# Kernel optimization log

Measured on AMD Instinct MI355X. Metric: run time of the kernel, lower is better.

The kernel has to match this reference:

```python
import jax, jax.numpy as jnp
import numpy as np

NUM_HEADS = 16
HEAD_SIZE = 64
D_MODEL = NUM_HEADS * HEAD_SIZE  # 1024


def setup_inputs() -> dict:
    key = jax.random.key(0)
    ks = jax.random.split(key, 12)
    B, S = 4, 2048
    q = jax.random.normal(ks[0], (B, S, D_MODEL), dtype=jnp.float32)
    k = jax.random.normal(ks[1], (B, S, D_MODEL), dtype=jnp.float32)
    v = jax.random.normal(ks[2], (B, S, D_MODEL), dtype=jnp.float32)
    w = jax.random.uniform(ks[3], (B, S), dtype=jnp.float32)
    scale = 1.0 / np.sqrt(D_MODEL)
    Wq = jax.random.normal(ks[4], (D_MODEL, D_MODEL), dtype=jnp.float32) * scale
    Wk = jax.random.normal(ks[5], (D_MODEL, D_MODEL), dtype=jnp.float32) * scale
    Wv = jax.random.normal(ks[6], (D_MODEL, D_MODEL), dtype=jnp.float32) * scale
    Wo = jax.random.normal(ks[7], (D_MODEL, D_MODEL), dtype=jnp.float32) * scale
    bq = jnp.zeros((D_MODEL,), jnp.float32)
    bk = jnp.zeros((D_MODEL,), jnp.float32)
    bv = jnp.zeros((D_MODEL,), jnp.float32)
    bo = jnp.zeros((D_MODEL,), jnp.float32)
    return {"q": q, "k": k, "v": v, "w": w,
            "Wq": Wq, "bq": bq, "Wk": Wk, "bk": bk,
            "Wv": Wv, "bv": bv, "Wo": Wo, "bo": bo}


def reference(q, k, v, w, Wq, bq, Wk, bk, Wv, bv, Wo, bo):
    B, S, _ = q.shape
    H, Dh = NUM_HEADS, HEAD_SIZE

    def split_heads(x):  # [B,S,D] -> [B,H,S,Dh]
        return x.reshape(B, -1, H, Dh).transpose(0, 2, 1, 3)

    q_h = split_heads(q @ Wq + bq)
    k_h = split_heads(k @ Wk + bk)
    v_h = split_heads(v @ Wv + bv)

    # [B,H,Sq,Sk]
    score = jnp.einsum('bhqd,bhkd->bhqk', q_h, k_h) / jnp.sqrt(
        jnp.asarray(Dh, jnp.float32))
    # weighted unnormalized softmax: exp(score)*w / sum (no max subtraction,
    # faithful to original)
    exp_score = jnp.exp(score) * w[:, None, None, :]
    attn = exp_score / (jnp.sum(exp_score, axis=-1, keepdims=True) + 1e-12)

    context = jnp.einsum('bhqk,bhkd->bhqd', attn, v_h)  # [B,H,S,Dh]
    context = context.transpose(0, 2, 1, 3).reshape(B, -1, H * Dh)
    return context @ Wo + bo
```

## Files before the change

### kernel.cpp

```cpp
#include <hip/hip_runtime.h>
#include <hip/hip_bf16.h>

typedef __bf16 bf16x8 __attribute__((ext_vector_type(8)));
typedef float f32x4 __attribute__((ext_vector_type(4)));
typedef float f32x8 __attribute__((ext_vector_type(8)));
typedef float f32x16 __attribute__((ext_vector_type(16)));
typedef unsigned short u16;
typedef unsigned int u32;

#define SB 4
#define SS 2048
#define SD 1024
#define SH 16
#define SDH 64

__device__ __forceinline__ u16 f2bf(float f) {
  union { float f; u32 u; } x; x.f = f;
  u32 r = (x.u + 0x7FFFu + ((x.u >> 16) & 1u)) >> 16;
  return (u16)r;
}

__device__ __forceinline__ void gl_lds16(const void* g, void* l) {
  __builtin_amdgcn_global_load_lds(
      (__attribute__((address_space(1))) void*)g,
      (__attribute__((address_space(3))) void*)l, 16, 0, 0);
}

__global__ void cast_bf16_kernel(const float* __restrict__ in,
                                 u32* __restrict__ out, int n8) {
  int i = blockIdx.x * blockDim.x + threadIdx.x;
  if (i >= n8) return;
  const float4* inp = (const float4*)in;
  float4 a = inp[2 * i], b = inp[2 * i + 1];
  uint4 o;
  asm("v_cvt_pk_bf16_f32 %0, %1, %2" : "=v"(o.x) : "v"(a.x), "v"(a.y));
  asm("v_cvt_pk_bf16_f32 %0, %1, %2" : "=v"(o.y) : "v"(a.z), "v"(a.w));
  asm("v_cvt_pk_bf16_f32 %0, %1, %2" : "=v"(o.z) : "v"(b.x), "v"(b.y));
  asm("v_cvt_pk_bf16_f32 %0, %1, %2" : "=v"(o.w) : "v"(b.z), "v"(b.w));
  ((uint4*)out)[i] = o;
}

__global__ void log2w_kernel(const float* __restrict__ w,
                             float* __restrict__ lwg) {
  int i = blockIdx.x * 256 + threadIdx.x;
  lwg[i] = __builtin_amdgcn_logf(w[i]);
}

__global__ void transpose_cast_kernel(const float* __restrict__ W0,
                                      const float* __restrict__ W1,
                                      const float* __restrict__ W2,
                                      const float* __restrict__ W3,
                                      u16* __restrict__ T0,
                                      u16* __restrict__ T1,
                                      u16* __restrict__ T2,
                                      u16* __restrict__ T3) {
  __shared__ float t[32][33];
  int z = blockIdx.z;
  const float* W = (z == 0) ? W0 : (z == 1) ? W1 : (z == 2) ? W2 : W3;
  u16* Wt = (z == 0) ? T0 : (z == 1) ? T1 : (z == 2) ? T2 : T3;
  int bx = blockIdx.x, by = blockIdx.y;
  int tx = threadIdx.x, ty = threadIdx.y;
#pragma unroll
  for (int j = 0; j < 32; j += 8)
    t[ty + j][tx] = W[(size_t)(by * 32 + ty + j) * SD + bx * 32 + tx];
  __syncthreads();
#pragma unroll
  for (int j = 0; j < 32; j += 8)
    Wt[(size_t)(bx * 32 + ty + j) * SD + by * 32 + tx] = f2bf(t[tx][ty + j]);
}

template <int MODE>
__global__ __launch_bounds__(256, 2)
void gemm_bt(const u16* __restrict__ A, const u16* __restrict__ Bt,
             const float* __restrict__ bias, void* __restrict__ Out,
             int M, int N, int K) {
  __shared__ u16 Asl[2][128 * 64];
  __shared__ u16 Bsl[2][128 * 64];
  const int ntile = N >> 7;
  int bid = blockIdx.x;
  bid = (bid & 7) * ((int)gridDim.x >> 3) + (bid >> 3);
  int m0 = (bid / ntile) * 128, n0 = (bid % ntile) * 128;
  int tid = threadIdx.x;
  int lane = tid & 63, wv = tid >> 6;
  int wr = wv >> 1, wc = wv & 1;

  auto stage = [&](int buf, int k0) {
#pragma unroll
    for (int it = 0; it < 4; ++it) {
      int c = tid + it * 256;
      int row = c >> 3, sl = c & 7;
      int ssl = sl ^ (row & 7);
      gl_lds16(A + (size_t)(m0 + row) * K + k0 + ssl * 8,
               (char*)&Asl[buf][0] + c * 16);
      gl_lds16(Bt + (size_t)(n0 + row) * K + k0 + ssl * 8,
               (char*)&Bsl[buf][0] + c * 16);
    }
  };

  f32x4 acc[4][4] = {};
  stage(0, 0);

  int nk = K >> 6;
  for (int kt = 0; kt < nk; ++kt) {
    int buf = kt & 1;
    if (kt + 1 < nk) {
      stage(buf ^ 1, (kt + 1) << 6);
      asm volatile("s_waitcnt vmcnt(8) lgkmcnt(0)" ::: "memory");
    } else {
      asm volatile("s_waitcnt vmcnt(0) lgkmcnt(0)" ::: "memory");
    }
    __builtin_amdgcn_s_barrier();
#pragma unroll
    for (int kk = 0; kk < 2; ++kk) {
      bf16x8 af[4], bfr[4];
#pragma unroll
      for (int i = 0; i < 4; ++i) {
        int ar = wr * 64 + i * 16 + (lane & 15);
        int abyt = (ar * 128 + (kk * 32 + (lane >> 4) * 8) * 2) ^
                   ((ar & 7) << 4);
        af[i] = *(const bf16x8*)((const char*)&Asl[buf][0] + abyt);
        int br = wc * 64 + i * 16 + (lane & 15);
        int bbyt = (br * 128 + (kk * 32 + (lane >> 4) * 8) * 2) ^
                   ((br & 7) << 4);
        bfr[i] = *(const bf16x8*)((const char*)&Bsl[buf][0] + bbyt);
      }
#pragma unroll
      for (int i = 0; i < 4; ++i)
#pragma unroll
        for (int j = 0; j < 4; ++j)
          acc[i][j] = __builtin_amdgcn_mfma_f32_16x16x32_bf16(
              af[i], bfr[j], acc[i][j], 0, 0, 0);
    }
    __builtin_amdgcn_s_barrier();
  }

  int cg = lane >> 4, cc = lane & 15;
#pragma unroll
  for (int i = 0; i < 4; ++i) {
#pragma unroll
    for (int j = 0; j < 4; ++j) {
#pragma unroll
      for (int r = 0; r < 4; ++r) {
        int m = m0 + wr * 64 + i * 16 + cg * 4 + r;
        int n = n0 + wc * 64 + j * 16 + cc;
        float val = acc[i][j][r];
        if (MODE == 0) {
          val = (val + bias[n]) * 0.18033688011112042f;
          int b = m >> 11, s = m & 2047, h = n >> 6, dh = n & 63;
          ((u16*)Out)[((size_t)((b * SH + h) * SS + s) << 6) + dh] = f2bf(val);
        } else if (MODE == 1) {
          val += bias[n];
          int b = m >> 11, s = m & 2047, h = n >> 6, dh = n & 63;
          size_t off = ((size_t)(b * SH + h) << 17) + ((size_t)(s >> 5) << 11) +
                       ((size_t)(dh >> 4) << 9) +
                       ((size_t)((s & 31) | ((dh & 8) << 2)) << 3) + (dh & 7);
          ((u16*)Out)[off] = f2bf(val);
        } else if (MODE == 2) {
          val += bias[m];
          int h = m >> 6, dh = m & 63, b = n >> 11, s = n & 2047;
          size_t off = ((size_t)(b * SH + h) << 17) + ((size_t)(s >> 4) << 10) +
                       ((size_t)(dh >> 5) << 9) +
                       ((size_t)(((s >> 3) & 1) * 32 + (dh & 31)) << 3) +
                       (s & 7);
          ((u16*)Out)[off] = f2bf(val);
        } else {
          val += bias[n];
          ((float*)Out)[(size_t)m * N + n] = val;
        }
      }
    }
  }
}

__global__ __launch_bounds__(256, 4)
void attn_kernel(const u16* __restrict__ Qh, const u16* __restrict__ Kf,
                 const u16* __restrict__ Vf, const float* __restrict__ lwg,
                 u16* __restrict__ Ctx) {
  __shared__ __align__(16) char smem[2][16384];

  int bid = blockIdx.x;
  int swz = (bid & 7) * 128 + (bid >> 3);
  int bh = swz >> 4;
  int qt = swz & 15;
  int b = bh >> 4, hh = bh & 15;
  int q0 = qt * 128;
  int tid = threadIdx.x, lane = tid & 63, qw = tid >> 6;
  int ql = lane & 31, h = lane >> 5;
  const size_t basebh = (size_t)bh * (SS * SDH);
  const char* Ksrc = (const char*)(Kf + basebh);
  const char* Vsrc = (const char*)(Vf + basebh);
  const float* lwp = lwg + b * SS;

  bf16x8 qf[4];
  {
    const u16* qp = Qh + basebh + (size_t)(q0 + qw * 32 + ql) * SDH + h * 8;
#pragma unroll
    for (int st = 0; st < 4; ++st) qf[st] = *(const bf16x8*)(qp + st * 16);
  }

  auto stage = [&](int s, int t) {
    char* dst = &smem[s][0];
#pragma unroll
    for (int it = 0; it < 4; ++it) {
      int c = tid + it * 256;
      gl_lds16((c < 512 ? Ksrc : Vsrc - 8192) + (size_t)t * 8192 + c * 16,
               dst + c * 16);
    }
  };

  f32x16 ctx0 = {}, ctx1 = {};
  float rs = 0.f;

  stage(0, 0);

  for (int t = 0; t < 32; ++t) {
    int s = t & 1;
    asm volatile("s_waitcnt vmcnt(0)" ::: "memory");
    __builtin_amdgcn_s_barrier();
    if (t + 1 < 32) stage(s ^ 1, t + 1);

    const char* Ks = &smem[s][0];
    const char* Vs = Ks + 8192;
    int kvb = t * 64;
    u32 pk[8][2];
#pragma unroll
    for (int kt = 0; kt < 2; ++kt) {
      bf16x8 kf[4];
#pragma unroll
      for (int st = 0; st < 4; ++st)
        kf[st] = *(const bf16x8*)(Ks + (kt * 4 + st) * 1024 + lane * 16);
      const float* lb = lwp + kvb + kt * 32 + h * 4;
      f32x4 l0 = *(const f32x4*)(lb);
      f32x4 l1 = *(const f32x4*)(lb + 8);
      f32x4 l2 = *(const f32x4*)(lb + 16);
      f32x4 l3 = *(const f32x4*)(lb + 24);
      f32x8 lo = __builtin_shufflevector(l0, l1, 0, 1, 2, 3, 4, 5, 6, 7);
      f32x8 hi = __builtin_shufflevector(l2, l3, 0, 1, 2, 3, 4, 5, 6, 7);
      f32x16 sc = __builtin_shufflevector(lo, hi, 0, 1, 2, 3, 4, 5, 6, 7, 8,
                                          9, 10, 11, 12, 13, 14, 15);
      __builtin_amdgcn_s_setprio(1);
#pragma unroll
      for (int st = 0; st < 4; ++st)
        sc = __builtin_amdgcn_mfma_f32_32x32x16_bf16(kf[st], qf[st], sc,
                                                     0, 0, 0);
      __builtin_amdgcn_s_setprio(0);
#pragma unroll
      for (int e2 = 0; e2 < 4; ++e2) {
        float v0 = __builtin_amdgcn_exp2f(sc[e2 * 4 + 0]);
        float v1 = __builtin_amdgcn_exp2f(sc[e2 * 4 + 1]);
        float v2 = __builtin_amdgcn_exp2f(sc[e2 * 4 + 2]);
        float v3 = __builtin_amdgcn_exp2f(sc[e2 * 4 + 3]);
        rs += (v0 + v1) + (v2 + v3);
        u32 p0, p1;
        asm("v_cvt_pk_bf16_f32 %0, %1, %2" : "=v"(p0) : "v"(v0), "v"(v1));
        asm("v_cvt_pk_bf16_f32 %0, %1, %2" : "=v"(p1) : "v"(v2), "v"(v3));
        pk[kt * 4 + e2][0] = p0;
        pk[kt * 4 + e2][1] = p1;
      }
    }
#pragma unroll
    for (int ksl = 0; ksl < 4; ++ksl) {
      bf16x8 vf0 = *(const bf16x8*)(Vs + (ksl * 2 + 0) * 1024 + lane * 16);
      bf16x8 vf1 = *(const bf16x8*)(Vs + (ksl * 2 + 1) * 1024 + lane * 16);
      u32 d0 = pk[2 * ksl][0], d1 = pk[2 * ksl][1];
      u32 s0 = pk[2 * ksl + 1][0], s1 = pk[2 * ksl + 1][1];
      asm("v_permlane32_swap_b32 %0, %1" : "+v"(d0), "+v"(s0));
      asm("v_permlane32_swap_b32 %0, %1" : "+v"(d1), "+v"(s1));
      union { u32 uu[4]; bf16x8 v; } pa;
      pa.uu[0] = d0; pa.uu[1] = d1; pa.uu[2] = s0; pa.uu[3] = s1;
      __builtin_amdgcn_s_setprio(1);
      ctx0 = __builtin_amdgcn_mfma_f32_32x32x16_bf16(pa.v, vf0, ctx0, 0, 0, 0);
      ctx1 = __builtin_amdgcn_mfma_f32_32x32x16_bf16(pa.v, vf1, ctx1, 0, 0, 0);
      __builtin_amdgcn_s_setprio(0);
    }
  }

  rs += __shfl_xor(rs, 32, 64);
  float rinv = 1.0f / (rs + 1e-12f);
#pragma unroll
  for (int reg = 0; reg < 16; ++reg) {
    int qrow = (reg & 3) + 8 * (reg >> 2) + 4 * h;
    float ri = __shfl(rinv, qrow, 64);
    int srow = q0 + qw * 32 + qrow;
    size_t base = ((size_t)(b * SS + srow) << 10) + hh * SDH;
    Ctx[base + ql] = f2bf(ctx0[reg] * ri);
    Ctx[base + 32 + ql] = f2bf(ctx1[reg] * ri);
  }
}

extern "C" void kernel_launch(void* const* d_in, const int* in_sizes, int n_in,
                              void* d_out, int out_size, void* d_ws,
                              size_t ws_size, hipStream_t stream) {
  const float* q = (const float*)d_in[0];
  const float* k = (const float*)d_in[1];
  const float* v = (const float*)d_in[2];
  const float* w = (const float*)d_in[3];
  const float* Wq = (const float*)d_in[4];
  const float* bq = (const float*)d_in[5];
  const float* Wk = (const float*)d_in[6];
  const float* bk = (const float*)d_in[7];
  const float* Wv = (const float*)d_in[8];
  const float* bv = (const float*)d_in[9];
  const float* Wo = (const float*)d_in[10];
  const float* bo = (const float*)d_in[11];
  float* out = (float*)d_out;

  char* ws = (char*)d_ws;
  const size_t SZ = (size_t)8192 * 1024 * 2;
  u16* qb = (u16*)(ws);
  u16* kb = (u16*)(ws + SZ);
  u16* vb = (u16*)(ws + 2 * SZ);
  u16* WqT = (u16*)(ws + 3 * SZ);
  u16* WkT = WqT + 1024 * 1024;
  u16* WvT = WkT + 1024 * 1024;
  u16* WoT = WvT + 1024 * 1024;
  u16* Qh = (u16*)(ws + 3 * SZ + (size_t)4 * 1024 * 1024 * 2);
  u16* Kf = Qh + (size_t)8192 * 1024;
  u16* Vf = Kf + (size_t)8192 * 1024;
  float* lwg = (float*)(ws + 3 * SZ + (size_t)4 * 1024 * 1024 * 2 +
                        (size_t)3 * 8192 * 1024 * 2);
  u16* Ctx = qb;

  cast_bf16_kernel<<<4096, 256, 0, stream>>>(q, (u32*)qb, 1048576);
  cast_bf16_kernel<<<4096, 256, 0, stream>>>(k, (u32*)kb, 1048576);
  cast_bf16_kernel<<<4096, 256, 0, stream>>>(v, (u32*)vb, 1048576);
  log2w_kernel<<<32, 256, 0, stream>>>(w, lwg);
  dim3 tb(32, 8), tg(32, 32, 4);
  transpose_cast_kernel<<<tg, tb, 0, stream>>>(Wq, Wk, Wv, Wo,
                                               WqT, WkT, WvT, WoT);

  gemm_bt<0><<<512, 256, 0, stream>>>(qb, WqT, bq, Qh, 8192, 1024, 1024);
  gemm_bt<1><<<512, 256, 0, stream>>>(kb, WkT, bk, Kf, 8192, 1024, 1024);
  gemm_bt<2><<<512, 256, 0, stream>>>(WvT, vb, bv, Vf, 1024, 8192, 1024);

  attn_kernel<<<1024, 256, 0, stream>>>(Qh, Kf, Vf, lwg, Ctx);

  gemm_bt<3><<<512, 256, 0, stream>>>(Ctx, WoT, bo, out, 8192, 1024, 1024);
}
```

Before: 222.4 us.

## Split K/V staging with finer waitcnt, cache log-weights in LDS, fuse casts

Splits the attention tile staging into separate K and V loads. The wait before the QK step now covers only the K tile, and V is waited on only before the PV step, so V loads overlap QK compute. The per-batch log2 weights are copied once into shared memory instead of being read from global memory every tile. The three fp32->bf16 cast launches are merged into one 3D-grid launch to cut launch overhead. LDS use grows by 8 KB per block, which may reduce occupancy, and the vmcnt counts depend on a fixed issue order of the async loads.

```diff
diff --git a/kernel.cpp b/kernel.cpp
--- a/kernel.cpp
+++ b/kernel.cpp
@@ -26,10 +26,15 @@
       (__attribute__((address_space(3))) void*)l, 16, 0, 0);
 }
 
-__global__ void cast_bf16_kernel(const float* __restrict__ in,
-                                 u32* __restrict__ out, int n8) {
-  int i = blockIdx.x * blockDim.x + threadIdx.x;
-  if (i >= n8) return;
+__global__ void cast3_kernel(const float* __restrict__ q,
+                             const float* __restrict__ k,
+                             const float* __restrict__ v,
+                             u32* __restrict__ oq, u32* __restrict__ ok,
+                             u32* __restrict__ ov) {
+  int sel = blockIdx.y;
+  const float* in = (sel == 0) ? q : (sel == 1) ? k : v;
+  u32* out = (sel == 0) ? oq : (sel == 1) ? ok : ov;
+  int i = blockIdx.x * 256 + threadIdx.x;
   const float4* inp = (const float4*)in;
   float4 a = inp[2 * i], b = inp[2 * i + 1];
   uint4 o;
@@ -176,7 +181,9 @@
 void attn_kernel(const u16* __restrict__ Qh, const u16* __restrict__ Kf,
                  const u16* __restrict__ Vf, const float* __restrict__ lwg,
                  u16* __restrict__ Ctx) {
-  __shared__ __align__(16) char smem[2][16384];
+  __shared__ u16 Kl[2][4096];
+  __shared__ u16 Vl[2][4096];
+  __shared__ float lwl[SS];
 
   int bid = blockIdx.x;
   int swz = (bid & 7) * 128 + (bid >> 3);
@@ -189,7 +196,14 @@
   const size_t basebh = (size_t)bh * (SS * SDH);
   const char* Ksrc = (const char*)(Kf + basebh);
   const char* Vsrc = (const char*)(Vf + basebh);
-  const float* lwp = lwg + b * SS;
+
+  {
+    const float4* src = (const float4*)(lwg + b * SS);
+    float4 r0 = src[tid];
+    float4 r1 = src[tid + 256];
+    ((float4*)lwl)[tid] = r0;
+    ((float4*)lwl)[tid + 256] = r1;
+  }
 
   bf16x8 qf[4];
   {
@@ -198,38 +212,31 @@
     for (int st = 0; st < 4; ++st) qf[st] = *(const bf16x8*)(qp + st * 16);
   }
 
-  auto stage = [&](int s, int t) {
-    char* dst = &smem[s][0];
-#pragma unroll
-    for (int it = 0; it < 4; ++it) {
-      int c = tid + it * 256;
-      gl_lds16((c < 512 ? Ksrc : Vsrc - 8192) + (size_t)t * 8192 + c * 16,
-               dst + c * 16);
-    }
+  auto stageK = [&](int s, int t) {
+    const char* p = Ksrc + (size_t)t * 8192;
+    gl_lds16(p + tid * 16, (char*)&Kl[s][0] + tid * 16);
+    gl_lds16(p + 4096 + tid * 16, (char*)&Kl[s][0] + 4096 + tid * 16);
+  };
+  auto stageV = [&](int s, int t) {
+    const char* p = Vsrc + (size_t)t * 8192;
+    gl_lds16(p + tid * 16, (char*)&Vl[s][0] + tid * 16);
+    gl_lds16(p + 4096 + tid * 16, (char*)&Vl[s][0] + 4096 + tid * 16);
   };
 
   f32x16 ctx0 = {}, ctx1 = {};
   float rs = 0.f;
-
-  stage(0, 0);
-
-  for (int t = 0; t < 32; ++t) {
-    int s = t & 1;
-    asm volatile("s_waitcnt vmcnt(0)" ::: "memory");
-    __builtin_amdgcn_s_barrier();
-    if (t + 1 < 32) stage(s ^ 1, t + 1);
-
-    const char* Ks = &smem[s][0];
-    const char* Vs = Ks + 8192;
+  u32 pk[8][2];
+
+  auto qk = [&](int t) {
+    const char* Ks = (const char*)&Kl[t & 1][0];
     int kvb = t * 64;
-    u32 pk[8][2];
 #pragma unroll
     for (int kt = 0; kt < 2; ++kt) {
       bf16x8 kf[4];
 #pragma unroll
       for (int st = 0; st < 4; ++st)
         kf[st] = *(const bf16x8*)(Ks + (kt * 4 + st) * 1024 + lane * 16);
-      const float* lb = lwp + kvb + kt * 32 + h * 4;
+      const float* lb = lwl + kvb + kt * 32 + h * 4;
       f32x4 l0 = *(const f32x4*)(lb);
       f32x4 l1 = *(const f32x4*)(lb + 8);
       f32x4 l2 = *(const f32x4*)(lb + 16);
@@ -258,6 +265,10 @@
         pk[kt * 4 + e2][1] = p1;
       }
     }
+  };
+
+  auto pv = [&](int t) {
+    const char* Vs = (const char*)&Vl[t & 1][0];
 #pragma unroll
     for (int ksl = 0; ksl < 4; ++ksl) {
       bf16x8 vf0 = *(const bf16x8*)(Vs + (ksl * 2 + 0) * 1024 + lane * 16);
@@ -273,7 +284,27 @@
       ctx1 = __builtin_amdgcn_mfma_f32_32x32x16_bf16(pa.v, vf1, ctx1, 0, 0, 0);
       __builtin_amdgcn_s_setprio(0);
     }
-  }
+  };
+
+  stageK(0, 0);
+  stageV(0, 0);
+  asm volatile("s_waitcnt lgkmcnt(0)" ::: "memory");
+  __builtin_amdgcn_s_barrier();
+
+  for (int t = 0; t < 31; ++t) {
+    asm volatile("s_waitcnt vmcnt(2)" ::: "memory");
+    __builtin_amdgcn_s_barrier();
+    stageK((t + 1) & 1, t + 1);
+    stageV((t + 1) & 1, t + 1);
+    qk(t);
+    asm volatile("s_waitcnt vmcnt(4)" ::: "memory");
+    pv(t);
+  }
+  asm volatile("s_waitcnt vmcnt(2)" ::: "memory");
+  __builtin_amdgcn_s_barrier();
+  qk(31);
+  asm volatile("s_waitcnt vmcnt(0)" ::: "memory");
+  pv(31);
 
   rs += __shfl_xor(rs, 32, 64);
   float rinv = 1.0f / (rs + 1e-12f);
@@ -321,9 +352,8 @@
                         (size_t)3 * 8192 * 1024 * 2);
   u16* Ctx = qb;
 
-  cast_bf16_kernel<<<4096, 256, 0, stream>>>(q, (u32*)qb, 1048576);
-  cast_bf16_kernel<<<4096, 256, 0, stream>>>(k, (u32*)kb, 1048576);
-  cast_bf16_kernel<<<4096, 256, 0, stream>>>(v, (u32*)vb, 1048576);
+  cast3_kernel<<<dim3(4096, 3), 256, 0, stream>>>(q, k, v, (u32*)qb,
+                                                  (u32*)kb, (u32*)vb);
   log2w_kernel<<<32, 256, 0, stream>>>(w, lwg);
   dim3 tb(32, 8), tg(32, 32, 4);
   transpose_cast_kernel<<<tg, tb, 0, stream>>>(Wq, Wk, Wv, Wo,
```

Result: faster. 214.3 us (-3.7%).
